# Performance work log

Measured on AMD Instinct MI355X. Metric: run time of the kernel, lower is better.

## Reference

```python
import jax, jax.numpy as jnp
import numpy as np

STEPS = 32768
D_IO = 63      # input/output feature size (hardcoded in module)
H = 256        # hidden_size
L = 6          # num_layers


def setup_inputs() -> dict:
    key = jax.random.key(0)
    ks = jax.random.split(key, 9)
    s = 1.0 / np.sqrt(H)
    inputs = jax.random.normal(ks[0], (STEPS, D_IO), dtype=jnp.float32)
    W_in = jax.random.uniform(ks[1], (H, D_IO), minval=-s, maxval=s, dtype=jnp.float32)
    b_in = jax.random.uniform(ks[2], (H,), minval=-s, maxval=s, dtype=jnp.float32)
    # PyTorch LSTM weights: per layer W_ih [4H, in], W_hh [4H, H], biases [4H].
    # Layer 0 input size == H (after the input Linear), so all layers share shape.
    W_ih = jax.random.uniform(ks[3], (L, 4 * H, H), minval=-s, maxval=s, dtype=jnp.float32)
    W_hh = jax.random.uniform(ks[4], (L, 4 * H, H), minval=-s, maxval=s, dtype=jnp.float32)
    b_ih = jax.random.uniform(ks[5], (L, 4 * H), minval=-s, maxval=s, dtype=jnp.float32)
    b_hh = jax.random.uniform(ks[6], (L, 4 * H), minval=-s, maxval=s, dtype=jnp.float32)
    W_fc = jax.random.uniform(ks[7], (D_IO, H), minval=-s, maxval=s, dtype=jnp.float32)
    b_fc = jax.random.uniform(ks[8], (D_IO,), minval=-s, maxval=s, dtype=jnp.float32)
    return {"inputs": inputs, "W_in": W_in, "b_in": b_in, "W_ih": W_ih,
            "W_hh": W_hh, "b_ih": b_ih, "b_hh": b_hh, "W_fc": W_fc, "b_fc": b_fc}


def _forward(inputs, W_in, b_in, W_ih, W_hh, b_ih, b_hh, W_fc, b_fc):
    # Original forward calls step(input, None) each timestep -> hidden state is
    # reset to zeros every step, so all timesteps are independent and can be
    # batched along the step axis.
    x = inputs @ W_in.T + b_in  # (S, H)
    h = x
    for l in range(L):
        h_prev = jnp.zeros_like(h)  # zero initial hidden state each step
        # gates: (S, 4H); h_prev @ W_hh kept for math-faithfulness to cuDNN step
        gates = h @ W_ih[l].T + h_prev @ W_hh[l].T + b_ih[l] + b_hh[l]
        i, f, g, o = jnp.split(gates, 4, axis=-1)  # torch gate order i,f,g,o
        c = jax.nn.sigmoid(i) * jnp.tanh(g)        # f * c_prev == 0
        h = jax.nn.sigmoid(o) * jnp.tanh(c)
    out = h @ W_fc.T + b_fc  # (S, 63)
    # matches the `outputs` buffer of shape (steps, 1, 63)
    return out[:, None, :]


def reference(inputs, W_in, b_in, W_ih, W_hh, b_ih, b_hh, W_fc, b_fc):
    return _forward(inputs, W_in, b_in, W_ih, W_hh, b_ih, b_hh, W_fc, b_fc)
```

## Files before the change

kernel.cpp:

```cpp
#include <hip/hip_runtime.h>

#define STEPS 32768
#define DIO 63
#define HSZ 256
#define NL 6
#define BM 64
#define THREADS 512

#define NBGF  (NL * 2 * 8 * 8 * 3 * 512)
#define NBIAS (NL * 768)
#define NBINF (16 * 2 * 64 * 8)
#define NBFCF (4 * 8 * 64 * 8)

typedef __bf16 bf16_8 __attribute__((ext_vector_type(8)));
typedef __bf16 bf16_4 __attribute__((ext_vector_type(4)));
typedef float f32x4 __attribute__((ext_vector_type(4)));

#define LOG2E  1.4426950408889634f
#define LOG2E2 2.8853900817779268f

__device__ __forceinline__ unsigned short f2bf(float f) {
    unsigned int u = __float_as_uint(f);
    u = u + 0x7fffu + ((u >> 16) & 1u);
    return (unsigned short)(u >> 16);
}

__global__ void prep_kernel(const float* __restrict__ W_in,
                            const float* __restrict__ W_ih,
                            const float* __restrict__ b_ih,
                            const float* __restrict__ b_hh,
                            const float* __restrict__ W_fc,
                            unsigned short* __restrict__ Bg,
                            float* __restrict__ bias,
                            unsigned short* __restrict__ Bin,
                            unsigned short* __restrict__ Bfc) {
    int idx = blockIdx.x * 256 + threadIdx.x;
    if (idx < NBGF) {
        int e    = idx & 7;
        int lane = (idx >> 3) & 63;
        int t    = idx >> 9;
        int g    = t % 3;
        int u    = t / 3;
        int kk   = u & 7;
        int v    = u >> 3;
        int w    = v & 7;
        int x    = v >> 3;
        int p    = x & 1;
        int l    = x >> 1;
        int f = (p * 8 + w) * 16 + (lane & 15);
        int k = kk * 32 + (lane >> 4) * 8 + e;
        int r = f + (g == 0 ? 0 : (g == 1 ? 512 : 768));
        float sc = (g == 1) ? LOG2E2 : LOG2E;
        Bg[idx] = f2bf(W_ih[((size_t)l * 1024 + r) * HSZ + k] * sc);
        return;
    }
    idx -= NBGF;
    if (idx < NBIAS) {
        int j = idx % 768, l = idx / 768;
        int g = j >> 8;
        int r = (j < 256) ? j : j + 256;
        float sc = (g == 1) ? LOG2E2 : LOG2E;
        bias[idx] = (b_ih[l * 1024 + r] + b_hh[l * 1024 + r]) * sc;
        return;
    }
    idx -= NBIAS;
    if (idx < NBINF) {
        int e = idx & 7, lane = (idx >> 3) & 63, kk = (idx >> 9) & 1, fb = idx >> 10;
        int f = fb * 16 + (lane & 15);
        int k = kk * 32 + (lane >> 4) * 8 + e;
        Bin[idx] = (k < DIO) ? f2bf(W_in[f * DIO + k]) : (unsigned short)0;
        return;
    }
    idx -= NBINF;
    if (idx < NBFCF) {
        int e = idx & 7, lane = (idx >> 3) & 63, kk = (idx >> 9) & 7, fm = idx >> 12;
        int f = fm * 16 + (lane & 15);
        int k = kk * 32 + (lane >> 4) * 8 + e;
        Bfc[idx] = (f < DIO) ? f2bf(W_fc[f * HSZ + k]) : (unsigned short)0;
    }
}

__global__ __launch_bounds__(THREADS, 2) void rnn_fused(
    const float* __restrict__ inp, const float* __restrict__ b_in,
    const float* __restrict__ b_fc,
    const unsigned short* __restrict__ Bg, const float* __restrict__ bias,
    const unsigned short* __restrict__ Bin, const unsigned short* __restrict__ Bfc,
    float* __restrict__ out) {
    __shared__ __align__(16) unsigned short h_lds[2 * 8 * 4 * 64 * 8];
    __shared__ __align__(16) unsigned short in_lds[2 * 4 * 64 * 8];

    const int tid = threadIdx.x;
    const int lane = tid & 63;
    const int l15 = lane & 15;
    const int lq = lane >> 4;
    const int wid = tid >> 6;
    const int row0 = blockIdx.x * BM;
    const int rdB = lq * 1024 + l15 * 16;

    for (int idx = tid; idx < BM * 64; idx += THREADS) {
        int s = idx >> 6, k = idx & 63;
        float v = (k < DIO) ? inp[(size_t)(row0 + s) * DIO + k] : 0.f;
        int off = (k >> 5) * 4096 + ((k >> 3) & 3) * 1024 + s * 16 + (k & 7) * 2;
        *(unsigned short*)((char*)in_lds + off) = f2bf(v);
    }
    __syncthreads();

    {
        f32x4 acc[2][4];
#pragma unroll
        for (int m = 0; m < 2; ++m) {
            f32x4 b4 = *(const f32x4*)(b_in + (2 * wid + m) * 16 + lq * 4);
#pragma unroll
            for (int n = 0; n < 4; ++n) acc[m][n] = b4;
        }
        const bf16_8* __restrict__ pA = (const bf16_8*)Bin + lane;
#pragma unroll
        for (int kk = 0; kk < 2; ++kk) {
            bf16_8 a[2], b[4];
#pragma unroll
            for (int m = 0; m < 2; ++m) a[m] = pA[((2 * wid + m) * 2 + kk) * 64];
#pragma unroll
            for (int n = 0; n < 4; ++n)
                b[n] = *(const bf16_8*)((const char*)in_lds + rdB + kk * 4096 + n * 256);
#pragma unroll
            for (int m = 0; m < 2; ++m)
#pragma unroll
                for (int n = 0; n < 4; ++n)
                    acc[m][n] = __builtin_amdgcn_mfma_f32_16x16x32_bf16(a[m], b[n], acc[m][n], 0, 0, 0);
        }
#pragma unroll
        for (int m = 0; m < 2; ++m) {
            int wb = wid * 4096 + (2 * m + (lq >> 1)) * 1024 + l15 * 16 + (lq & 1) * 8;
#pragma unroll
            for (int n = 0; n < 4; ++n) {
                bf16_4 hv;
#pragma unroll
                for (int r = 0; r < 4; ++r) hv[r] = (__bf16)acc[m][n][r];
                *(bf16_4*)((char*)h_lds + wb + n * 256) = hv;
            }
        }
    }
    __syncthreads();

    for (int l = 0; l < NL; ++l) {
        const char* cur = (const char*)h_lds + (l & 1) * 32768;
        char* nxt = (char*)h_lds + ((l + 1) & 1) * 32768;
#pragma unroll
        for (int pi = 0; pi < 2; ++pi) {
            const int p = pi ^ (wid & 1);
            const int fb = p * 8 + wid;
            const float* bb = bias + l * 768 + fb * 16 + lq * 4;
            f32x4 ai[4], ag[4], ao[4];
            {
                f32x4 bi4 = *(const f32x4*)(bb);
                f32x4 bg4 = *(const f32x4*)(bb + 256);
                f32x4 bo4 = *(const f32x4*)(bb + 512);
#pragma unroll
                for (int n = 0; n < 4; ++n) { ai[n] = bi4; ag[n] = bg4; ao[n] = bo4; }
            }
            const bf16_8* __restrict__ pW =
                (const bf16_8*)Bg + (size_t)((l * 2 + p) * 8 + wid) * 1536 + lane;
#pragma unroll
            for (int kk = 0; kk < 8; ++kk) {
                bf16_8 wa = pW[kk * 192];
                bf16_8 wg = pW[kk * 192 + 64];
                bf16_8 wo = pW[kk * 192 + 128];
                bf16_8 b[4];
#pragma unroll
                for (int n = 0; n < 4; ++n)
                    b[n] = *(const bf16_8*)(cur + rdB + kk * 4096 + n * 256);
#pragma unroll
                for (int n = 0; n < 4; ++n) {
                    ai[n] = __builtin_amdgcn_mfma_f32_16x16x32_bf16(wa, b[n], ai[n], 0, 0, 0);
                    ag[n] = __builtin_amdgcn_mfma_f32_16x16x32_bf16(wg, b[n], ag[n], 0, 0, 0);
                    ao[n] = __builtin_amdgcn_mfma_f32_16x16x32_bf16(wo, b[n], ao[n], 0, 0, 0);
                }
            }
            const int wrp = (fb >> 1) * 4096 + ((fb & 1) * 2 + (lq >> 1)) * 1024 +
                            l15 * 16 + (lq & 1) * 8;
#pragma unroll
            for (int n = 0; n < 4; ++n) {
                bf16_4 hv;
#pragma unroll
                for (int r = 0; r < 4; ++r) {
                    float ei = __builtin_amdgcn_exp2f(fminf(ai[n][r], 34.f));
                    float eg = __builtin_amdgcn_exp2f(fminf(ag[n][r], 60.f));
                    float eo = __builtin_amdgcn_exp2f(fminf(ao[n][r], 34.f));
                    float c = ei * (eg - 1.f) *
                              __builtin_amdgcn_rcpf((1.f + ei) * (1.f + eg));
                    float z = c * c;
                    float tn = fmaf(z + 105.f, z, 945.f);
                    float td = fmaf(fmaf(15.f, z, 420.f), z, 945.f);
                    hv[r] = (__bf16)(eo * c * tn *
                                     __builtin_amdgcn_rcpf((1.f + eo) * td));
                }
                *(bf16_4*)(nxt + wrp + n * 256) = hv;
            }
        }
        __syncthreads();
    }

    {
        const char* cur = (const char*)h_lds;
        const int fm = wid & 3;
        const int sb = (wid >> 2) * 2;
        f32x4 o4[2];
#pragma unroll
        for (int n = 0; n < 2; ++n) o4[n] = (f32x4){0.f, 0.f, 0.f, 0.f};
        const bf16_8* __restrict__ pF = (const bf16_8*)Bfc + lane;
#pragma unroll
        for (int kk = 0; kk < 8; ++kk) {
            bf16_8 a = pF[(fm * 8 + kk) * 64];
#pragma unroll
            for (int n = 0; n < 2; ++n) {
                bf16_8 b = *(const bf16_8*)(cur + rdB + kk * 4096 + (sb + n) * 256);
                o4[n] = __builtin_amdgcn_mfma_f32_16x16x32_bf16(a, b, o4[n], 0, 0, 0);
            }
        }
#pragma unroll
        for (int n = 0; n < 2; ++n) {
            int s = row0 + (sb + n) * 16 + l15;
#pragma unroll
            for (int r = 0; r < 4; ++r) {
                int f = fm * 16 + lq * 4 + r;
                if (f < DIO) out[(size_t)s * DIO + f] = o4[n][r] + b_fc[f];
            }
        }
    }
}

extern "C" void kernel_launch(void* const* d_in, const int* in_sizes, int n_in,
                              void* d_out, int out_size, void* d_ws, size_t ws_size,
                              hipStream_t stream) {
    const float* inputs = (const float*)d_in[0];
    const float* W_in   = (const float*)d_in[1];
    const float* b_in   = (const float*)d_in[2];
    const float* W_ih   = (const float*)d_in[3];
    const float* b_ih   = (const float*)d_in[5];
    const float* b_hh   = (const float*)d_in[6];
    const float* W_fc   = (const float*)d_in[7];
    const float* b_fc   = (const float*)d_in[8];

    unsigned short* Bg  = (unsigned short*)d_ws;
    float* bias         = (float*)((char*)d_ws + (size_t)NBGF * 2);
    unsigned short* Bin = (unsigned short*)((char*)bias + (size_t)NBIAS * 4);
    unsigned short* Bfc = Bin + NBINF;

    int total = NBGF + NBIAS + NBINF + NBFCF;
    prep_kernel<<<(total + 255) / 256, 256, 0, stream>>>(W_in, W_ih, b_ih, b_hh, W_fc,
                                                         Bg, bias, Bin, Bfc);
    rnn_fused<<<STEPS / BM, THREADS, 0, stream>>>(inputs, b_in, b_fc, Bg, bias, Bin, Bfc,
                                                  (float*)d_out);
}
```

Measured before the change: 104.9 us.

## Switch to 32x32x16 MFMA tiles with per-wave 32-feature gate blocks

Replaces the 16x16x32 MFMA tiling with 32x32x16 MFMAs, re-laying out the prepacked weights, biases and input/FC matrices for the new operand layout. Each wave now owns one 32-feature block across all 64 rows and computes the input and g gates first, then the output gate, which shortens live accumulator ranges. The input staging buffer is aliased into the second half of the h buffer to cut shared memory, the b_in bias moves into the prepacked bias array, and the tanh rational approximation is made cheaper with the exp clamps dropped. This trades fewer, larger MFMA issues and higher LDS operand reuse against lower approximation accuracy and possible overflow without the clamps.

```diff
diff --git a/kernel.cpp b/kernel.cpp
--- a/kernel.cpp
+++ b/kernel.cpp
@@ -7,14 +7,15 @@
 #define BM 64
 #define THREADS 512
 
-#define NBGF  (NL * 2 * 8 * 8 * 3 * 512)
-#define NBIAS (NL * 768)
-#define NBINF (16 * 2 * 64 * 8)
-#define NBFCF (4 * 8 * 64 * 8)
+#define NBGF  (NL * 8 * 16 * 3 * 512)
+#define NBIAS (19 * 256)
+#define NBINF (8 * 4 * 512)
+#define NBFCF (2 * 16 * 512)
 
 typedef __bf16 bf16_8 __attribute__((ext_vector_type(8)));
 typedef __bf16 bf16_4 __attribute__((ext_vector_type(4)));
 typedef float f32x4 __attribute__((ext_vector_type(4)));
+typedef float f32x16 __attribute__((ext_vector_type(16)));
 
 #define LOG2E  1.4426950408889634f
 #define LOG2E2 2.8853900817779268f
@@ -27,28 +28,26 @@
 
 __global__ void prep_kernel(const float* __restrict__ W_in,
                             const float* __restrict__ W_ih,
+                            const float* __restrict__ b_in,
                             const float* __restrict__ b_ih,
                             const float* __restrict__ b_hh,
                             const float* __restrict__ W_fc,
                             unsigned short* __restrict__ Bg,
-                            float* __restrict__ bias,
+                            float* __restrict__ biasF,
                             unsigned short* __restrict__ Bin,
                             unsigned short* __restrict__ Bfc) {
     int idx = blockIdx.x * 256 + threadIdx.x;
     if (idx < NBGF) {
         int e    = idx & 7;
         int lane = (idx >> 3) & 63;
-        int t    = idx >> 9;
-        int g    = t % 3;
-        int u    = t / 3;
-        int kk   = u & 7;
-        int v    = u >> 3;
-        int w    = v & 7;
-        int x    = v >> 3;
-        int p    = x & 1;
-        int l    = x >> 1;
-        int f = (p * 8 + w) * 16 + (lane & 15);
-        int k = kk * 32 + (lane >> 4) * 8 + e;
+        int rest = idx >> 9;
+        int g    = rest % 3;
+        int t    = rest / 3;
+        int kk   = t & 15;
+        int fb   = (t >> 4) & 7;
+        int l    = t >> 7;
+        int f = fb * 32 + (lane & 31);
+        int k = kk * 16 + (lane >> 5) * 8 + e;
         int r = f + (g == 0 ? 0 : (g == 1 ? 512 : 768));
         float sc = (g == 1) ? LOG2E2 : LOG2E;
         Bg[idx] = f2bf(W_ih[((size_t)l * 1024 + r) * HSZ + k] * sc);
@@ -56,175 +55,191 @@
     }
     idx -= NBGF;
     if (idx < NBIAS) {
-        int j = idx % 768, l = idx / 768;
-        int g = j >> 8;
-        int r = (j < 256) ? j : j + 256;
-        float sc = (g == 1) ? LOG2E2 : LOG2E;
-        bias[idx] = (b_ih[l * 1024 + r] + b_hh[l * 1024 + r]) * sc;
+        int j  = idx & 3;
+        int hi = (idx >> 2) & 1;
+        int q  = (idx >> 3) & 3;
+        int wi = (idx >> 5) & 7;
+        int lg = idx >> 8;
+        int f = wi * 32 + q * 8 + hi * 4 + j;
+        float val;
+        if (lg == 18) {
+            val = b_in[f];
+        } else {
+            int l = lg / 3, g = lg % 3;
+            int r = f + (g == 0 ? 0 : (g == 1 ? 512 : 768));
+            float sc = (g == 1) ? LOG2E2 : LOG2E;
+            val = (b_ih[l * 1024 + r] + b_hh[l * 1024 + r]) * sc;
+        }
+        biasF[idx] = val;
         return;
     }
     idx -= NBIAS;
     if (idx < NBINF) {
-        int e = idx & 7, lane = (idx >> 3) & 63, kk = (idx >> 9) & 1, fb = idx >> 10;
-        int f = fb * 16 + (lane & 15);
-        int k = kk * 32 + (lane >> 4) * 8 + e;
+        int e = idx & 7, lane = (idx >> 3) & 63, kk = (idx >> 9) & 3, fb = idx >> 11;
+        int f = fb * 32 + (lane & 31);
+        int k = kk * 16 + (lane >> 5) * 8 + e;
         Bin[idx] = (k < DIO) ? f2bf(W_in[f * DIO + k]) : (unsigned short)0;
         return;
     }
     idx -= NBINF;
     if (idx < NBFCF) {
-        int e = idx & 7, lane = (idx >> 3) & 63, kk = (idx >> 9) & 7, fm = idx >> 12;
-        int f = fm * 16 + (lane & 15);
-        int k = kk * 32 + (lane >> 4) * 8 + e;
+        int e = idx & 7, lane = (idx >> 3) & 63, kk = (idx >> 9) & 15, ff = idx >> 13;
+        int f = ff * 32 + (lane & 31);
+        int k = kk * 16 + (lane >> 5) * 8 + e;
         Bfc[idx] = (f < DIO) ? f2bf(W_fc[f * HSZ + k]) : (unsigned short)0;
     }
 }
 
+__device__ __forceinline__ f32x16 bias16(const float* pb) {
+    f32x4 a = *(const f32x4*)pb;
+    f32x4 b = *(const f32x4*)(pb + 8);
+    f32x4 c = *(const f32x4*)(pb + 16);
+    f32x4 d = *(const f32x4*)(pb + 24);
+    f32x16 r;
+    r[0]=a[0]; r[1]=a[1]; r[2]=a[2]; r[3]=a[3];
+    r[4]=b[0]; r[5]=b[1]; r[6]=b[2]; r[7]=b[3];
+    r[8]=c[0]; r[9]=c[1]; r[10]=c[2]; r[11]=c[3];
+    r[12]=d[0]; r[13]=d[1]; r[14]=d[2]; r[15]=d[3];
+    return r;
+}
+
+__device__ __forceinline__ void write16(char* buf, int wid, int hi, int l31,
+                                        int sp, f32x16 v) {
+    int base = wid * 4096 + (sp * 32 + l31) * 16 + hi * 8;
+#pragma unroll
+    for (int q = 0; q < 4; ++q) {
+        bf16_4 hv;
+#pragma unroll
+        for (int j = 0; j < 4; ++j) hv[j] = (__bf16)v[q * 4 + j];
+        *(bf16_4*)(buf + base + q * 1024) = hv;
+    }
+}
+
+__device__ __forceinline__ void hact_write(char* buf, int wid, int hi, int l31,
+                                           int sp, f32x16 ao, f32x16 cv) {
+    int base = wid * 4096 + (sp * 32 + l31) * 16 + hi * 8;
+#pragma unroll
+    for (int q = 0; q < 4; ++q) {
+        bf16_4 hv;
+#pragma unroll
+        for (int j = 0; j < 4; ++j) {
+            int r = q * 4 + j;
+            float eo = __builtin_amdgcn_exp2f(ao[r]);
+            float c = cv[r];
+            float z = c * c;
+            float num = eo * c * (z + 15.f);
+            float den = (1.f + eo) * fmaf(6.f, z, 15.f);
+            hv[j] = (__bf16)(num * __builtin_amdgcn_rcpf(den));
+        }
+        *(bf16_4*)(buf + base + q * 1024) = hv;
+    }
+}
+
 __global__ __launch_bounds__(THREADS, 2) void rnn_fused(
-    const float* __restrict__ inp, const float* __restrict__ b_in,
-    const float* __restrict__ b_fc,
-    const unsigned short* __restrict__ Bg, const float* __restrict__ bias,
+    const float* __restrict__ inp, const float* __restrict__ b_fc,
+    const unsigned short* __restrict__ Bg, const float* __restrict__ biasF,
     const unsigned short* __restrict__ Bin, const unsigned short* __restrict__ Bfc,
     float* __restrict__ out) {
     __shared__ __align__(16) unsigned short h_lds[2 * 8 * 4 * 64 * 8];
-    __shared__ __align__(16) unsigned short in_lds[2 * 4 * 64 * 8];
+    unsigned short* in_alias = h_lds + 16384;
 
     const int tid = threadIdx.x;
     const int lane = tid & 63;
-    const int l15 = lane & 15;
-    const int lq = lane >> 4;
+    const int l31 = lane & 31;
+    const int hi = lane >> 5;
     const int wid = tid >> 6;
     const int row0 = blockIdx.x * BM;
-    const int rdB = lq * 1024 + l15 * 16;
+    const int vB = hi * 1024 + l31 * 16;
 
     for (int idx = tid; idx < BM * 64; idx += THREADS) {
         int s = idx >> 6, k = idx & 63;
         float v = (k < DIO) ? inp[(size_t)(row0 + s) * DIO + k] : 0.f;
         int off = (k >> 5) * 4096 + ((k >> 3) & 3) * 1024 + s * 16 + (k & 7) * 2;
-        *(unsigned short*)((char*)in_lds + off) = f2bf(v);
+        *(unsigned short*)((char*)in_alias + off) = f2bf(v);
     }
     __syncthreads();
 
     {
-        f32x4 acc[2][4];
-#pragma unroll
-        for (int m = 0; m < 2; ++m) {
-            f32x4 b4 = *(const f32x4*)(b_in + (2 * wid + m) * 16 + lq * 4);
-#pragma unroll
-            for (int n = 0; n < 4; ++n) acc[m][n] = b4;
-        }
-        const bf16_8* __restrict__ pA = (const bf16_8*)Bin + lane;
-#pragma unroll
-        for (int kk = 0; kk < 2; ++kk) {
-            bf16_8 a[2], b[4];
-#pragma unroll
-            for (int m = 0; m < 2; ++m) a[m] = pA[((2 * wid + m) * 2 + kk) * 64];
-#pragma unroll
-            for (int n = 0; n < 4; ++n)
-                b[n] = *(const bf16_8*)((const char*)in_lds + rdB + kk * 4096 + n * 256);
-#pragma unroll
-            for (int m = 0; m < 2; ++m)
-#pragma unroll
-                for (int n = 0; n < 4; ++n)
-                    acc[m][n] = __builtin_amdgcn_mfma_f32_16x16x32_bf16(a[m], b[n], acc[m][n], 0, 0, 0);
-        }
-#pragma unroll
-        for (int m = 0; m < 2; ++m) {
-            int wb = wid * 4096 + (2 * m + (lq >> 1)) * 1024 + l15 * 16 + (lq & 1) * 8;
-#pragma unroll
-            for (int n = 0; n < 4; ++n) {
-                bf16_4 hv;
-#pragma unroll
-                for (int r = 0; r < 4; ++r) hv[r] = (__bf16)acc[m][n][r];
-                *(bf16_4*)((char*)h_lds + wb + n * 256) = hv;
-            }
-        }
+        const char* pA = (const char*)Bin + lane * 16;
+        const char* cin = (const char*)in_alias;
+        f32x16 x0 = bias16(biasF + (18 * 8 + wid) * 32 + hi * 4);
+        f32x16 x1 = x0;
+#pragma unroll
+        for (int kk = 0; kk < 4; ++kk) {
+            bf16_8 wa = *(const bf16_8*)(pA + (wid * 4 + kk) * 1024);
+            bf16_8 b0 = *(const bf16_8*)(cin + vB + (kk >> 1) * 4096 + (kk & 1) * 2048);
+            bf16_8 b1 = *(const bf16_8*)(cin + vB + (kk >> 1) * 4096 + (kk & 1) * 2048 + 512);
+            x0 = __builtin_amdgcn_mfma_f32_32x32x16_bf16(wa, b0, x0, 0, 0, 0);
+            x1 = __builtin_amdgcn_mfma_f32_32x32x16_bf16(wa, b1, x1, 0, 0, 0);
+        }
+        write16((char*)h_lds, wid, hi, l31, 0, x0);
+        write16((char*)h_lds, wid, hi, l31, 1, x1);
     }
     __syncthreads();
 
+    const char* BgW = (const char*)Bg + (size_t)wid * 49152 + lane * 16;
     for (int l = 0; l < NL; ++l) {
         const char* cur = (const char*)h_lds + (l & 1) * 32768;
         char* nxt = (char*)h_lds + ((l + 1) & 1) * 32768;
-#pragma unroll
-        for (int pi = 0; pi < 2; ++pi) {
-            const int p = pi ^ (wid & 1);
-            const int fb = p * 8 + wid;
-            const float* bb = bias + l * 768 + fb * 16 + lq * 4;
-            f32x4 ai[4], ag[4], ao[4];
-            {
-                f32x4 bi4 = *(const f32x4*)(bb);
-                f32x4 bg4 = *(const f32x4*)(bb + 256);
-                f32x4 bo4 = *(const f32x4*)(bb + 512);
-#pragma unroll
-                for (int n = 0; n < 4; ++n) { ai[n] = bi4; ag[n] = bg4; ao[n] = bo4; }
-            }
-            const bf16_8* __restrict__ pW =
-                (const bf16_8*)Bg + (size_t)((l * 2 + p) * 8 + wid) * 1536 + lane;
-#pragma unroll
-            for (int kk = 0; kk < 8; ++kk) {
-                bf16_8 wa = pW[kk * 192];
-                bf16_8 wg = pW[kk * 192 + 64];
-                bf16_8 wo = pW[kk * 192 + 128];
-                bf16_8 b[4];
-#pragma unroll
-                for (int n = 0; n < 4; ++n)
-                    b[n] = *(const bf16_8*)(cur + rdB + kk * 4096 + n * 256);
-#pragma unroll
-                for (int n = 0; n < 4; ++n) {
-                    ai[n] = __builtin_amdgcn_mfma_f32_16x16x32_bf16(wa, b[n], ai[n], 0, 0, 0);
-                    ag[n] = __builtin_amdgcn_mfma_f32_16x16x32_bf16(wg, b[n], ag[n], 0, 0, 0);
-                    ao[n] = __builtin_amdgcn_mfma_f32_16x16x32_bf16(wo, b[n], ao[n], 0, 0, 0);
-                }
-            }
-            const int wrp = (fb >> 1) * 4096 + ((fb & 1) * 2 + (lq >> 1)) * 1024 +
-                            l15 * 16 + (lq & 1) * 8;
-#pragma unroll
-            for (int n = 0; n < 4; ++n) {
-                bf16_4 hv;
-#pragma unroll
-                for (int r = 0; r < 4; ++r) {
-                    float ei = __builtin_amdgcn_exp2f(fminf(ai[n][r], 34.f));
-                    float eg = __builtin_amdgcn_exp2f(fminf(ag[n][r], 60.f));
-                    float eo = __builtin_amdgcn_exp2f(fminf(ao[n][r], 34.f));
-                    float c = ei * (eg - 1.f) *
-                              __builtin_amdgcn_rcpf((1.f + ei) * (1.f + eg));
-                    float z = c * c;
-                    float tn = fmaf(z + 105.f, z, 945.f);
-                    float td = fmaf(fmaf(15.f, z, 420.f), z, 945.f);
-                    hv[r] = (__bf16)(eo * c * tn *
-                                     __builtin_amdgcn_rcpf((1.f + eo) * td));
-                }
-                *(bf16_4*)(nxt + wrp + n * 256) = hv;
-            }
-        }
+        const char* pW = BgW + (size_t)l * 393216;
+        const float* pb = biasF + (l * 3 * 8 + wid) * 32 + hi * 4;
+
+        f32x16 ai0 = bias16(pb), ai1 = ai0;
+        f32x16 ag0 = bias16(pb + 256), ag1 = ag0;
+#pragma unroll
+        for (int kk = 0; kk < 16; ++kk) {
+            bf16_8 wa = *(const bf16_8*)(pW + (kk * 3 + 0) * 1024);
+            bf16_8 wg = *(const bf16_8*)(pW + (kk * 3 + 1) * 1024);
+            bf16_8 b0 = *(const bf16_8*)(cur + vB + (kk >> 1) * 4096 + (kk & 1) * 2048);
+            bf16_8 b1 = *(const bf16_8*)(cur + vB + (kk >> 1) * 4096 + (kk & 1) * 2048 + 512);
+            ai0 = __builtin_amdgcn_mfma_f32_32x32x16_bf16(wa, b0, ai0, 0, 0, 0);
+            ai1 = __builtin_amdgcn_mfma_f32_32x32x16_bf16(wa, b1, ai1, 0, 0, 0);
+            ag0 = __builtin_amdgcn_mfma_f32_32x32x16_bf16(wg, b0, ag0, 0, 0, 0);
+            ag1 = __builtin_amdgcn_mfma_f32_32x32x16_bf16(wg, b1, ag1, 0, 0, 0);
+        }
+        f32x16 c0, c1;
+#pragma unroll
+        for (int r = 0; r < 16; ++r) {
+            float ei = __builtin_amdgcn_exp2f(ai0[r]);
+            float eg = __builtin_amdgcn_exp2f(ag0[r]);
+            c0[r] = ei * (eg - 1.f) * __builtin_amdgcn_rcpf((1.f + ei) * (1.f + eg));
+            ei = __builtin_amdgcn_exp2f(ai1[r]);
+            eg = __builtin_amdgcn_exp2f(ag1[r]);
+            c1[r] = ei * (eg - 1.f) * __builtin_amdgcn_rcpf((1.f + ei) * (1.f + eg));
+        }
+        f32x16 ao0 = bias16(pb + 512), ao1 = ao0;
+#pragma unroll
+        for (int kk = 0; kk < 16; ++kk) {
+            bf16_8 wo = *(const bf16_8*)(pW + (kk * 3 + 2) * 1024);
+            bf16_8 b0 = *(const bf16_8*)(cur + vB + (kk >> 1) * 4096 + (kk & 1) * 2048);
+            bf16_8 b1 = *(const bf16_8*)(cur + vB + (kk >> 1) * 4096 + (kk & 1) * 2048 + 512);
+            ao0 = __builtin_amdgcn_mfma_f32_32x32x16_bf16(wo, b0, ao0, 0, 0, 0);
+            ao1 = __builtin_amdgcn_mfma_f32_32x32x16_bf16(wo, b1, ao1, 0, 0, 0);
+        }
+        hact_write(nxt, wid, hi, l31, 0, ao0, c0);
+        hact_write(nxt, wid, hi, l31, 1, ao1, c1);
         __syncthreads();
     }
 
-    {
+    if (wid < 4) {
+        const int ff = wid & 1;
+        const int sf = wid >> 1;
+        const char* pF = (const char*)Bfc + lane * 16;
         const char* cur = (const char*)h_lds;
-        const int fm = wid & 3;
-        const int sb = (wid >> 2) * 2;
-        f32x4 o4[2];
-#pragma unroll
-        for (int n = 0; n < 2; ++n) o4[n] = (f32x4){0.f, 0.f, 0.f, 0.f};
-        const bf16_8* __restrict__ pF = (const bf16_8*)Bfc + lane;
-#pragma unroll
-        for (int kk = 0; kk < 8; ++kk) {
-            bf16_8 a = pF[(fm * 8 + kk) * 64];
-#pragma unroll
-            for (int n = 0; n < 2; ++n) {
-                bf16_8 b = *(const bf16_8*)(cur + rdB + kk * 4096 + (sb + n) * 256);
-                o4[n] = __builtin_amdgcn_mfma_f32_16x16x32_bf16(a, b, o4[n], 0, 0, 0);
-            }
-        }
-#pragma unroll
-        for (int n = 0; n < 2; ++n) {
-            int s = row0 + (sb + n) * 16 + l15;
-#pragma unroll
-            for (int r = 0; r < 4; ++r) {
-                int f = fm * 16 + lq * 4 + r;
-                if (f < DIO) out[(size_t)s * DIO + f] = o4[n][r] + b_fc[f];
-            }
+        f32x16 o;
+#pragma unroll
+        for (int r = 0; r < 16; ++r) o[r] = 0.f;
+#pragma unroll
+        for (int kk = 0; kk < 16; ++kk) {
+            bf16_8 a = *(const bf16_8*)(pF + (ff * 16 + kk) * 1024);
+            bf16_8 b = *(const bf16_8*)(cur + vB + (kk >> 1) * 4096 + (kk & 1) * 2048 + sf * 512);
+            o = __builtin_amdgcn_mfma_f32_32x32x16_bf16(a, b, o, 0, 0, 0);
+        }
+        int s = row0 + sf * 32 + l31;
+#pragma unroll
+        for (int r = 0; r < 16; ++r) {
+            int f = ff * 32 + (r & 3) + 8 * (r >> 2) + 4 * hi;
+            if (f < DIO) out[(size_t)s * DIO + f] = o[r] + b_fc[f];
         }
     }
 }
@@ -242,13 +257,13 @@
     const float* b_fc   = (const float*)d_in[8];
 
     unsigned short* Bg  = (unsigned short*)d_ws;
-    float* bias         = (float*)((char*)d_ws + (size_t)NBGF * 2);
-    unsigned short* Bin = (unsigned short*)((char*)bias + (size_t)NBIAS * 4);
+    float* biasF        = (float*)((char*)d_ws + (size_t)NBGF * 2);
+    unsigned short* Bin = (unsigned short*)((char*)biasF + (size_t)NBIAS * 4);
     unsigned short* Bfc = Bin + NBINF;
 
     int total = NBGF + NBIAS + NBINF + NBFCF;
-    prep_kernel<<<(total + 255) / 256, 256, 0, stream>>>(W_in, W_ih, b_ih, b_hh, W_fc,
-                                                         Bg, bias, Bin, Bfc);
-    rnn_fused<<<STEPS / BM, THREADS, 0, stream>>>(inputs, b_in, b_fc, Bg, bias, Bin, Bfc,
+    prep_kernel<<<(total + 255) / 256, 256, 0, stream>>>(W_in, W_ih, b_in, b_ih, b_hh,
+                                                         W_fc, Bg, biasF, Bin, Bfc);
+    rnn_fused<<<STEPS / BM, THREADS, 0, stream>>>(inputs, b_fc, Bg, biasF, Bin, Bfc,
                                                   (float*)d_out);
 }
```

After: 179.4 us. 1.71x slower.

## Software-pipeline gate weight loads across k-steps and passes, alias input LDS

Applied to the files above, without the earlier changes.

Gate weight fragments are now prefetched one k-step ahead, and the first fragment of the next pass or layer is loaded during the last k-step of the current one. This hides global-load latency behind the MFMA work. The separate input LDS buffer is dropped and aliased onto the second half of the h buffer to cut LDS usage. The activation also changes: the exp2 clamps are removed and a lower-order rational tanh approximation is used, which lowers ALU cost but risks accuracy and inf/NaN on large pre-activations.

```diff
diff --git a/kernel.cpp b/kernel.cpp
--- a/kernel.cpp
+++ b/kernel.cpp
@@ -80,6 +80,65 @@
     }
 }
 
+__device__ __forceinline__ void ld3(const char* p, bf16_8& a, bf16_8& g, bf16_8& o) {
+    a = *(const bf16_8*)(p);
+    g = *(const bf16_8*)(p + 1024);
+    o = *(const bf16_8*)(p + 2048);
+}
+
+__device__ __forceinline__ void gate_pass(
+    const char* pW, const char* pNext,
+    bf16_8& wa0, bf16_8& wg0, bf16_8& wo0,
+    const char* cur, int rdB, const float* pb,
+    f32x4 (&ai)[4], f32x4 (&ag)[4], f32x4 (&ao)[4]) {
+    f32x4 bi4 = *(const f32x4*)(pb);
+    f32x4 bg4 = *(const f32x4*)(pb + 256);
+    f32x4 bo4 = *(const f32x4*)(pb + 512);
+#pragma unroll
+    for (int n = 0; n < 4; ++n) { ai[n] = bi4; ag[n] = bg4; ao[n] = bo4; }
+    bf16_8 wa = wa0, wg = wg0, wo = wo0;
+#pragma unroll
+    for (int kk = 0; kk < 8; ++kk) {
+        bf16_8 na, ng, no;
+        if (kk < 7) ld3(pW + (kk + 1) * 3072, na, ng, no);
+        else        ld3(pNext, na, ng, no);
+        bf16_8 b[4];
+#pragma unroll
+        for (int n = 0; n < 4; ++n)
+            b[n] = *(const bf16_8*)(cur + rdB + kk * 4096 + n * 256);
+#pragma unroll
+        for (int n = 0; n < 4; ++n) {
+            ai[n] = __builtin_amdgcn_mfma_f32_16x16x32_bf16(wa, b[n], ai[n], 0, 0, 0);
+            ag[n] = __builtin_amdgcn_mfma_f32_16x16x32_bf16(wg, b[n], ag[n], 0, 0, 0);
+            ao[n] = __builtin_amdgcn_mfma_f32_16x16x32_bf16(wo, b[n], ao[n], 0, 0, 0);
+        }
+        wa = na; wg = ng; wo = no;
+    }
+    wa0 = wa; wg0 = wg; wo0 = wo;
+}
+
+__device__ __forceinline__ void act_write(char* nxt, int fb, int lq, int l15,
+                                          f32x4 (&ai)[4], f32x4 (&ag)[4], f32x4 (&ao)[4]) {
+    const int wrp = (fb >> 1) * 4096 + ((fb & 1) * 2 + (lq >> 1)) * 1024 +
+                    l15 * 16 + (lq & 1) * 8;
+#pragma unroll
+    for (int n = 0; n < 4; ++n) {
+        bf16_4 hv;
+#pragma unroll
+        for (int r = 0; r < 4; ++r) {
+            float ei = __builtin_amdgcn_exp2f(ai[n][r]);
+            float eg = __builtin_amdgcn_exp2f(ag[n][r]);
+            float eo = __builtin_amdgcn_exp2f(ao[n][r]);
+            float c = ei * (eg - 1.f) *
+                      __builtin_amdgcn_rcpf((1.f + ei) * (1.f + eg));
+            float z = c * c;
+            hv[r] = (__bf16)(eo * c * (z + 15.f) *
+                             __builtin_amdgcn_rcpf((1.f + eo) * fmaf(6.f, z, 15.f)));
+        }
+        *(bf16_4*)(nxt + wrp + n * 256) = hv;
+    }
+}
+
 __global__ __launch_bounds__(THREADS, 2) void rnn_fused(
     const float* __restrict__ inp, const float* __restrict__ b_in,
     const float* __restrict__ b_fc,
@@ -87,7 +146,7 @@
     const unsigned short* __restrict__ Bin, const unsigned short* __restrict__ Bfc,
     float* __restrict__ out) {
     __shared__ __align__(16) unsigned short h_lds[2 * 8 * 4 * 64 * 8];
-    __shared__ __align__(16) unsigned short in_lds[2 * 4 * 64 * 8];
+    unsigned short* in_alias = h_lds + 16384;
 
     const int tid = threadIdx.x;
     const int lane = tid & 63;
@@ -97,11 +156,17 @@
     const int row0 = blockIdx.x * BM;
     const int rdB = lq * 1024 + l15 * 16;
 
+    const char* Wb = (const char*)Bg + lane * 16;
+    const int pA = wid & 1, pB = 1 - pA;
+
+    bf16_8 wa0, wg0, wo0;
+    ld3(Wb + (size_t)(pA * 8 + wid) * 24576, wa0, wg0, wo0);
+
     for (int idx = tid; idx < BM * 64; idx += THREADS) {
         int s = idx >> 6, k = idx & 63;
         float v = (k < DIO) ? inp[(size_t)(row0 + s) * DIO + k] : 0.f;
         int off = (k >> 5) * 4096 + ((k >> 3) & 3) * 1024 + s * 16 + (k & 7) * 2;
-        *(unsigned short*)((char*)in_lds + off) = f2bf(v);
+        *(unsigned short*)((char*)in_alias + off) = f2bf(v);
     }
     __syncthreads();
 
@@ -113,15 +178,15 @@
 #pragma unroll
             for (int n = 0; n < 4; ++n) acc[m][n] = b4;
         }
-        const bf16_8* __restrict__ pA = (const bf16_8*)Bin + lane;
+        const bf16_8* __restrict__ pIA = (const bf16_8*)Bin + lane;
 #pragma unroll
         for (int kk = 0; kk < 2; ++kk) {
             bf16_8 a[2], b[4];
 #pragma unroll
-            for (int m = 0; m < 2; ++m) a[m] = pA[((2 * wid + m) * 2 + kk) * 64];
+            for (int m = 0; m < 2; ++m) a[m] = pIA[((2 * wid + m) * 2 + kk) * 64];
 #pragma unroll
             for (int n = 0; n < 4; ++n)
-                b[n] = *(const bf16_8*)((const char*)in_lds + rdB + kk * 4096 + n * 256);
+                b[n] = *(const bf16_8*)((const char*)in_alias + rdB + kk * 4096 + n * 256);
 #pragma unroll
             for (int m = 0; m < 2; ++m)
 #pragma unroll
@@ -145,58 +210,20 @@
     for (int l = 0; l < NL; ++l) {
         const char* cur = (const char*)h_lds + (l & 1) * 32768;
         char* nxt = (char*)h_lds + ((l + 1) & 1) * 32768;
-#pragma unroll
-        for (int pi = 0; pi < 2; ++pi) {
-            const int p = pi ^ (wid & 1);
-            const int fb = p * 8 + wid;
-            const float* bb = bias + l * 768 + fb * 16 + lq * 4;
-            f32x4 ai[4], ag[4], ao[4];
-            {
-                f32x4 bi4 = *(const f32x4*)(bb);
-                f32x4 bg4 = *(const f32x4*)(bb + 256);
-                f32x4 bo4 = *(const f32x4*)(bb + 512);
-#pragma unroll
-                for (int n = 0; n < 4; ++n) { ai[n] = bi4; ag[n] = bg4; ao[n] = bo4; }
-            }
-            const bf16_8* __restrict__ pW =
-                (const bf16_8*)Bg + (size_t)((l * 2 + p) * 8 + wid) * 1536 + lane;
-#pragma unroll
-            for (int kk = 0; kk < 8; ++kk) {
-                bf16_8 wa = pW[kk * 192];
-                bf16_8 wg = pW[kk * 192 + 64];
-                bf16_8 wo = pW[kk * 192 + 128];
-                bf16_8 b[4];
-#pragma unroll
-                for (int n = 0; n < 4; ++n)
-                    b[n] = *(const bf16_8*)(cur + rdB + kk * 4096 + n * 256);
-#pragma unroll
-                for (int n = 0; n < 4; ++n) {
-                    ai[n] = __builtin_amdgcn_mfma_f32_16x16x32_bf16(wa, b[n], ai[n], 0, 0, 0);
-                    ag[n] = __builtin_amdgcn_mfma_f32_16x16x32_bf16(wg, b[n], ag[n], 0, 0, 0);
-                    ao[n] = __builtin_amdgcn_mfma_f32_16x16x32_bf16(wo, b[n], ao[n], 0, 0, 0);
-                }
-            }
-            const int wrp = (fb >> 1) * 4096 + ((fb & 1) * 2 + (lq >> 1)) * 1024 +
-                            l15 * 16 + (lq & 1) * 8;
-#pragma unroll
-            for (int n = 0; n < 4; ++n) {
-                bf16_4 hv;
-#pragma unroll
-                for (int r = 0; r < 4; ++r) {
-                    float ei = __builtin_amdgcn_exp2f(fminf(ai[n][r], 34.f));
-                    float eg = __builtin_amdgcn_exp2f(fminf(ag[n][r], 60.f));
-                    float eo = __builtin_amdgcn_exp2f(fminf(ao[n][r], 34.f));
-                    float c = ei * (eg - 1.f) *
-                              __builtin_amdgcn_rcpf((1.f + ei) * (1.f + eg));
-                    float z = c * c;
-                    float tn = fmaf(z + 105.f, z, 945.f);
-                    float td = fmaf(fmaf(15.f, z, 420.f), z, 945.f);
-                    hv[r] = (__bf16)(eo * c * tn *
-                                     __builtin_amdgcn_rcpf((1.f + eo) * td));
-                }
-                *(bf16_4*)(nxt + wrp + n * 256) = hv;
-            }
-        }
+        const char* pWA = Wb + (size_t)((l * 2 + pA) * 8 + wid) * 24576;
+        const char* pWB = Wb + (size_t)((l * 2 + pB) * 8 + wid) * 24576;
+        const char* pWN = (l < NL - 1)
+            ? Wb + (size_t)(((l + 1) * 2 + pA) * 8 + wid) * 24576
+            : pWB;
+        const float* bl = bias + l * 768 + lq * 4;
+
+        f32x4 ai[4], ag[4], ao[4];
+        gate_pass(pWA, pWB, wa0, wg0, wo0, cur, rdB,
+                  bl + (pA * 8 + wid) * 16, ai, ag, ao);
+        act_write(nxt, pA * 8 + wid, lq, l15, ai, ag, ao);
+        gate_pass(pWB, pWN, wa0, wg0, wo0, cur, rdB,
+                  bl + (pB * 8 + wid) * 16, ai, ag, ao);
+        act_write(nxt, pB * 8 + wid, lq, l15, ai, ag, ao);
         __syncthreads();
     }
 
```

Result: slower. 115.2 us (+9.8%).
